# Performance work log

Hardware: AMD Instinct MI355X
Metric: run time of the kernel (lower is better)

## Reference

```python
import jax, jax.numpy as jnp
import numpy as np

FC = 16  # feat_channel
EPS = 1e-4


def _sch_forward(sch_feat, conv_weight, mask, target, pre_ind, ind):
    B, C, H, W = sch_feat.shape
    M = pre_ind.shape[1]
    fc = FC
    # _tranpose_and_gather_feat: gather per-object weight vectors at pre_ind
    cw = conv_weight.reshape(B, conv_weight.shape[1], H * W)          # B,Wt,HW
    weight = jnp.take_along_axis(cw, pre_ind[:, None, :], axis=2)    # B,Wt,M
    weight = jnp.transpose(weight, (0, 2, 1))                         # B,M,Wt
    # split into the 3-layer dynamic MLP params
    s1 = (fc + 2) * fc
    w1 = weight[..., :s1].reshape(B, M, fc, fc + 2)
    b1 = weight[..., s1:s1 + fc]
    s2 = s1 + fc
    w2 = weight[..., s2:s2 + fc * fc].reshape(B, M, fc, fc)
    b2 = weight[..., s2 + fc * fc:s2 + fc * fc + fc]
    s3 = s2 + fc * fc + fc
    w3 = weight[..., s3:s3 + fc]                                      # B,M,fc (1 out channel)
    b3 = weight[..., s3 + fc:s3 + fc + 1]                             # B,M,1
    # relative coordinate grids; note torch: x = pre_ind % w (int), y = pre_ind / w (true div)
    x = (pre_ind % W).astype(jnp.float32)
    y = pre_ind.astype(jnp.float32) / W
    xg = jnp.arange(W, dtype=jnp.float32)
    yg = jnp.arange(H, dtype=jnp.float32)
    x_rel = (xg[None, None, None, :] - x[:, :, None, None]) / 128.0   # B,M,1,W
    y_rel = (yg[None, None, :, None] - y[:, :, None, None]) / 128.0   # B,M,H,1
    x_rel = jnp.broadcast_to(x_rel, (B, M, H, W))
    y_rel = jnp.broadcast_to(y_rel, (B, M, H, W))
    feat = jnp.concatenate([
        jnp.broadcast_to(sch_feat[:, None], (B, M, C, H, W)),
        x_rel[:, :, None], y_rel[:, :, None]], axis=2)                # B,M,fc+2,H,W
    # three grouped 1x1 convs == per-instance matmuls
    h = jax.nn.relu(jnp.einsum('bmchw,bmoc->bmohw', feat, w1) + b1[:, :, :, None, None])
    h = jax.nn.relu(jnp.einsum('bmchw,bmoc->bmohw', h, w2) + b2[:, :, :, None, None])
    hm = jnp.einsum('bmchw,bmc->bmhw', h, w3) + b3[:, :, :, None]      # B,M,H,W
    hm = jnp.clip(jax.nn.sigmoid(hm), EPS, 1.0 - EPS)                  # _sigmoid
    # FastFocalLoss over (B*M, 1, H, W) with cat = 0
    neg_loss = jnp.sum(jnp.log(1.0 - hm) * hm ** 2 * (1.0 - target) ** 4)
    hm_flat = hm.reshape(B, M, H * W)
    pos_pred = jnp.take_along_axis(hm_flat, ind[..., None], axis=2)[..., 0]  # B,M
    pos_loss = jnp.sum(jnp.log(pos_pred) * (1.0 - pos_pred) ** 2 * mask)
    num_pos = jnp.sum(mask)
    loss = jnp.where(num_pos == 0,
                     -neg_loss,
                     -(pos_loss + neg_loss) / jnp.maximum(num_pos, 1.0))
    return loss


def setup_inputs() -> dict:
    key = jax.random.key(0)
    k1, k2, k3, k4, k5 = jax.random.split(key, 5)
    B, M, H, W = 4, 32, 152, 272
    Wt = (FC + 2) * FC + FC + FC * FC + FC + FC + 1  # 593
    return {
        'sch_feat': jax.random.normal(k1, (B, FC, H, W), dtype=jnp.float32),
        'conv_weight': jax.random.normal(k2, (B, Wt, H, W), dtype=jnp.float32),
        'mask': jnp.ones((B, M), dtype=jnp.float32),
        'pre_ind': jax.random.randint(k3, (B, M), 0, H * W, dtype=jnp.int64) if jax.config.jax_enable_x64 else jax.random.randint(k3, (B, M), 0, H * W).astype(jnp.int32),
        'target': jax.random.uniform(k4, (B, M, H, W), dtype=jnp.float32),
        'ind': jax.random.randint(k5, (B, M), 0, H * W).astype(jnp.int32),
    }


def reference(sch_feat, conv_weight, mask, pre_ind, target, ind):
    return _sch_forward(sch_feat, conv_weight, mask, target, pre_ind, ind)
```

## Files before the change

kernel.cpp:

```cpp
#include <hip/hip_runtime.h>

typedef unsigned int uint;
typedef unsigned short ushort;

constexpr int Bc = 4, Mc = 32, Hc = 152, Wc = 272;
constexpr int HWc = Hc * Wc;
constexpr int WTc = 593;
constexpr int NB = 8;
constexpr int NEG_BLOCKS = Bc * Mc * NB;
constexpr int ITERS = HWc / 64;
constexpr int POS_OFF = 1024;
constexpr int WC_OFF = 2048;
constexpr int WC_STRIDE = 600;
constexpr int APK1_OFF = WC_OFF + 128 * WC_STRIDE;
constexpr int APK2_OFF = APK1_OFF + 128 * 64 * 4;
constexpr size_t XOFF_BYTES = (size_t)(APK2_OFF + 128 * 64 * 4) * 4;
constexpr int CH = 24;
constexpr int XCVT_BLOCKS = 162 * Bc;

using f32x4 = __attribute__((ext_vector_type(4))) float;
using bf16x8 = __attribute__((ext_vector_type(8))) short;

__device__ inline uint pkbf(float lo, float hi) {
  uint r;
  asm("v_cvt_pk_bf16_f32 %0, %1, %2" : "=v"(r) : "v"(lo), "v"(hi));
  return r;
}
__device__ inline float bpermf(int byteaddr, float v) {
  return __int_as_float(__builtin_amdgcn_ds_bpermute(byteaddr, __float_as_int(v)));
}
__device__ inline uint bpermu(int byteaddr, uint v) {
  return (uint)__builtin_amdgcn_ds_bpermute(byteaddr, (int)v);
}

union FR { uint u[4]; bf16x8 v; };

__global__ __launch_bounds__(256) void fused_pre(const float* __restrict__ sf_all,
                                                 const float* __restrict__ cw,
                                                 const int* __restrict__ pre_ind,
                                                 const int* __restrict__ ind,
                                                 const float* __restrict__ mask,
                                                 ushort* __restrict__ xb,
                                                 float* __restrict__ ws) {
  __shared__ float sw[WTc];
  const int blk = blockIdx.x, tid = threadIdx.x;

  if (blk < XCVT_BLOCKS) {
    const int b = blk / 162, bx = blk - b * 162;
    const int px = bx * 256 + tid;
    if (px < HWc) {
      const float* s = sf_all + (size_t)b * 16 * HWc + px;
      uint q[8];
#pragma unroll
      for (int i = 0; i < 8; i++) q[i] = pkbf(s[(size_t)(2 * i) * HWc], s[(size_t)(2 * i + 1) * HWc]);
      const int hh = px / Wc, xx = px - hh * Wc;
      const uint q8 = pkbf((float)xx * 0.0078125f, (float)hh * 0.0078125f);
      uint4* dst = (uint4*)(xb + ((size_t)b * HWc + px) * CH);
      dst[0] = make_uint4(q[0], q[1], q[2], q[3]);
      dst[1] = make_uint4(q[4], q[5], q[6], q[7]);
      dst[2] = make_uint4(q8, 0u, 0u, 0u);
    }
    if (blk == 0 && tid < 32) ((uint*)(xb + (size_t)Bc * HWc * CH))[tid] = 0;
    return;
  }

  const int bm = blk - XCVT_BLOCKS, b = bm >> 5;
  const int p = pre_ind[bm];
  const float* wcol = cw + (size_t)b * WTc * HWc + p;
  float* wc = ws + WC_OFF + bm * WC_STRIDE;
  for (int j = tid; j < WTc; j += 256) {
    float v = wcol[(size_t)j * HWc];
    sw[j] = v;
    wc[j] = v;
  }
  __syncthreads();

  if (tid < 64) {
    const int g = tid >> 4, o = tid & 15;
    float a1f[8], a2f[8];
#pragma unroll
    for (int e = 0; e < 8; e++) {
      int k = 8 * g + e;
      a1f[e] = (k < 18) ? sw[o * 18 + k] : 0.0f;
      a2f[e] = (k < 16) ? sw[304 + o * 16 + k] : 0.0f;
    }
    uint4 u1, u2;
    u1.x = pkbf(a1f[0], a1f[1]); u1.y = pkbf(a1f[2], a1f[3]);
    u1.z = pkbf(a1f[4], a1f[5]); u1.w = pkbf(a1f[6], a1f[7]);
    u2.x = pkbf(a2f[0], a2f[1]); u2.y = pkbf(a2f[2], a2f[3]);
    u2.z = pkbf(a2f[4], a2f[5]); u2.w = pkbf(a2f[6], a2f[7]);
    ((uint4*)(ws + APK1_OFF))[bm * 64 + tid] = u1;
    ((uint4*)(ws + APK2_OFF))[bm * 64 + tid] = u2;
  } else if (tid == 64) {
    const float* sf = sf_all + (size_t)b * 16 * HWc;
    const int pi = ind[bm];
    float f[18];
#pragma unroll
    for (int c = 0; c < 16; c++) f[c] = sf[(size_t)c * HWc + pi];
    const int hh = pi / Wc;
    const float x0 = (float)(p % Wc);
    const float y0 = (float)p / (float)Wc;
    f[16] = ((float)(pi - hh * Wc) - x0) * 0.0078125f;
    f[17] = ((float)hh - y0) * 0.0078125f;
    float h1[16];
    for (int oo = 0; oo < 16; oo++) {
      float a = sw[288 + oo];
#pragma unroll
      for (int c = 0; c < 18; c++) a = fmaf(sw[oo * 18 + c], f[c], a);
      h1[oo] = fmaxf(a, 0.0f);
    }
    float h2[16];
    for (int oo = 0; oo < 16; oo++) {
      float a = sw[560 + oo];
#pragma unroll
      for (int c = 0; c < 16; c++) a = fmaf(sw[304 + oo * 16 + c], h1[c], a);
      h2[oo] = fmaxf(a, 0.0f);
    }
    float zv = sw[592];
#pragma unroll
    for (int c = 0; c < 16; c++) zv = fmaf(sw[576 + c], h2[c], zv);
    float hm = __fdividef(1.0f, 1.0f + __expf(-zv));
    hm = fminf(fmaxf(hm, 1e-4f), 1.0f - 1e-4f);
    const float om = 1.0f - hm;
    ws[POS_OFF + bm] = __logf(hm) * om * om * mask[bm];
  }
}

__global__ __launch_bounds__(256, 4) void sch_neg(const float* __restrict__ target,
                                                  const ushort* __restrict__ xbf,
                                                  const int* __restrict__ pre_ind,
                                                  float* __restrict__ ws) {
  const int tid = threadIdx.x;
  const int lane = tid & 63;
  const int wid = tid >> 6;
  const int xcd = blockIdx.x & 7;
  const int slot = blockIdx.x >> 3;
  const int b = xcd >> 1;
  const int m = slot & 31;
  const int nb = ((slot >> 5) << 1) | (xcd & 1);
  const int bm = (b << 5) | m;
  const int g = lane >> 4;
  const int o = lane & 15;

  const int p = pre_ind[bm];
  const float x0 = (float)(p % Wc);
  const float y0 = (float)p / (float)Wc;

  FR A1, A2;
  {
    uint4 u1 = ((const uint4*)(ws + APK1_OFF))[bm * 64 + lane];
    uint4 u2 = ((const uint4*)(ws + APK2_OFF))[bm * 64 + lane];
    A1.u[0] = u1.x; A1.u[1] = u1.y; A1.u[2] = u1.z; A1.u[3] = u1.w;
    A2.u[0] = u2.x; A2.u[1] = u2.y; A2.u[2] = u2.z; A2.u[3] = u2.w;
  }
  const float* wc = ws + WC_OFF + bm * WC_STRIDE;
  f32x4 c1v, c2v;
  float w3r[4];
#pragma unroll
  for (int r = 0; r < 4; r++) {
    int row = 4 * g + r;
    c1v[r] = wc[288 + row] - (wc[row * 18 + 16] * x0 + wc[row * 18 + 17] * y0) * 0.0078125f;
    c2v[r] = wc[560 + row];
    w3r[r] = wc[576 + row];
  }
  const float b3 = wc[592];

  const ushort* xb = xbf + (size_t)b * HWc * CH;
  const float* tg = target + (size_t)bm * HWc;

  const int aX16 = (lane ^ 16) << 2;
  const int aX32 = (lane ^ 32) << 2;
  const int aS0 = (o + ((g == 1) ? 32 : 0)) << 2;
  const int aS1 = (o + ((g == 1) ? 48 : 16)) << 2;

  float acc = 0.0f;
  const int gw = nb * 4 + wid;
  for (int it = gw; it < ITERS; it += 32) {
    const int base = it * 64;
    uint4 ld[4];
#pragma unroll
    for (int c = 0; c < 4; c++)
      ld[c] = *(const uint4*)(xb + (size_t)(base + 16 * c + o) * CH + g * 8);
    const float tval = tg[base + lane];

    float zpv[4];
#pragma unroll
    for (int half = 0; half < 2; half++) {
      FR B1a, B1b;
      B1a.u[0] = ld[2 * half].x; B1a.u[1] = ld[2 * half].y;
      B1a.u[2] = ld[2 * half].z; B1a.u[3] = ld[2 * half].w;
      B1b.u[0] = ld[2 * half + 1].x; B1b.u[1] = ld[2 * half + 1].y;
      B1b.u[2] = ld[2 * half + 1].z; B1b.u[3] = ld[2 * half + 1].w;
      f32x4 d1a = __builtin_amdgcn_mfma_f32_16x16x32_bf16(A1.v, B1a.v, c1v, 0, 0, 0);
      f32x4 d1b = __builtin_amdgcn_mfma_f32_16x16x32_bf16(A1.v, B1b.v, c1v, 0, 0, 0);
      uint pa0 = pkbf(fmaxf(d1a[0], 0.0f), fmaxf(d1a[1], 0.0f));
      uint pa1 = pkbf(fmaxf(d1a[2], 0.0f), fmaxf(d1a[3], 0.0f));
      uint pb0 = pkbf(fmaxf(d1b[0], 0.0f), fmaxf(d1b[1], 0.0f));
      uint pb1 = pkbf(fmaxf(d1b[2], 0.0f), fmaxf(d1b[3], 0.0f));
      FR B2a, B2b;
      B2a.u[0] = bpermu(aS0, pa0); B2a.u[1] = bpermu(aS0, pa1);
      B2a.u[2] = bpermu(aS1, pa0); B2a.u[3] = bpermu(aS1, pa1);
      B2b.u[0] = bpermu(aS0, pb0); B2b.u[1] = bpermu(aS0, pb1);
      B2b.u[2] = bpermu(aS1, pb0); B2b.u[3] = bpermu(aS1, pb1);
      f32x4 d2a = __builtin_amdgcn_mfma_f32_16x16x32_bf16(A2.v, B2a.v, c2v, 0, 0, 0);
      f32x4 d2b = __builtin_amdgcn_mfma_f32_16x16x32_bf16(A2.v, B2b.v, c2v, 0, 0, 0);
      zpv[2 * half] = fmaxf(d2a[0], 0.0f) * w3r[0] + fmaxf(d2a[1], 0.0f) * w3r[1] +
                      fmaxf(d2a[2], 0.0f) * w3r[2] + fmaxf(d2a[3], 0.0f) * w3r[3];
      zpv[2 * half + 1] = fmaxf(d2b[0], 0.0f) * w3r[0] + fmaxf(d2b[1], 0.0f) * w3r[1] +
                          fmaxf(d2b[2], 0.0f) * w3r[2] + fmaxf(d2b[3], 0.0f) * w3r[3];
    }
    const int b0 = g & 1, b1 = g & 2;
    const float pk_g  = b1 ? (b0 ? zpv[3] : zpv[2]) : (b0 ? zpv[1] : zpv[0]);
    const float pk_g1 = b1 ? (b0 ? zpv[2] : zpv[3]) : (b0 ? zpv[0] : zpv[1]);
    const float pk_g2 = b1 ? (b0 ? zpv[1] : zpv[0]) : (b0 ? zpv[3] : zpv[2]);
    const float pk_g3 = b1 ? (b0 ? zpv[0] : zpv[1]) : (b0 ? zpv[2] : zpv[3]);
    const float tA = pk_g + bpermf(aX16, pk_g1);
    const float tB = pk_g2 + bpermf(aX16, pk_g3);
    const float S = tA + bpermf(aX32, tB);

    const float zz = S + b3;
    float hm = __fdividef(1.0f, 1.0f + __expf(-zz));
    hm = fminf(fmaxf(hm, 1e-4f), 1.0f - 1e-4f);
    const float u = 1.0f - tval;
    const float u2 = u * u;
    acc += __logf(1.0f - hm) * hm * hm * (u2 * u2);
  }

  __shared__ float red[256];
  red[tid] = acc;
  __syncthreads();
  for (int s = 128; s > 0; s >>= 1) {
    if (tid < s) red[tid] += red[tid + s];
    __syncthreads();
  }
  if (tid == 0) ws[blockIdx.x] = red[0];
}

__global__ __launch_bounds__(256) void sch_final(const float* __restrict__ ws,
                                                 const float* __restrict__ mask,
                                                 float* __restrict__ out) {
  __shared__ float red[256];
  const int t = threadIdx.x;

  float s = 0.0f;
  for (int i = t; i < NEG_BLOCKS; i += 256) s += ws[i];
  red[t] = s; __syncthreads();
  for (int k = 128; k > 0; k >>= 1) { if (t < k) red[t] += red[t + k]; __syncthreads(); }
  const float neg = red[0];
  __syncthreads();

  float pv = (t < Bc * Mc) ? ws[POS_OFF + t] : 0.0f;
  red[t] = pv; __syncthreads();
  for (int k = 128; k > 0; k >>= 1) { if (t < k) red[t] += red[t + k]; __syncthreads(); }
  const float pos = red[0];
  __syncthreads();

  float mv = (t < Bc * Mc) ? mask[t] : 0.0f;
  red[t] = mv; __syncthreads();
  for (int k = 128; k > 0; k >>= 1) { if (t < k) red[t] += red[t + k]; __syncthreads(); }

  if (t == 0) {
    float np = red[0];
    out[0] = (np == 0.0f) ? (-neg) : (-(pos + neg) / fmaxf(np, 1.0f));
  }
}

extern "C" void kernel_launch(void* const* d_in, const int* in_sizes, int n_in,
                              void* d_out, int out_size, void* d_ws, size_t ws_size,
                              hipStream_t stream) {
  const float* sch_feat    = (const float*)d_in[0];
  const float* conv_weight = (const float*)d_in[1];
  const float* mask        = (const float*)d_in[2];
  const int*   pre_ind     = (const int*)d_in[3];
  const float* target      = (const float*)d_in[4];
  const int*   ind         = (const int*)d_in[5];
  float* out = (float*)d_out;
  float* ws  = (float*)d_ws;
  ushort* xbf = (ushort*)((char*)d_ws + XOFF_BYTES);

  fused_pre<<<dim3(XCVT_BLOCKS + Bc * Mc), dim3(256), 0, stream>>>(
      sch_feat, conv_weight, pre_ind, ind, mask, xbf, ws);
  sch_neg<<<dim3(NEG_BLOCKS), dim3(256), 0, stream>>>(target, xbf, pre_ind, ws);
  sch_final<<<dim3(1), dim3(256), 0, stream>>>(ws, mask, out);
}
```

Baseline: 49.16 us.

## Use grouped 16-pixel feature layout and software-prefetch next iteration loads

Reorganizes the bf16 feature buffer from per-pixel 48-byte records into 16-pixel groups, with channel halves and the coordinate channel stored contiguously, so each lane's load is coalesced and the padding lanes skip loads entirely. It also double-buffers the feature and target loads so the next iteration's data is fetched while the current one computes through the MFMA chain. The cost is extra registers for the prefetch buffers, which may affect occupancy under the 4-wave launch bound. Lanes in group 3 now read zeros and group 2 sees only the coordinate word, which must match the A-matrix packing.

```diff
diff --git a/kernel.cpp b/kernel.cpp
--- a/kernel.cpp
+++ b/kernel.cpp
@@ -2,6 +2,7 @@
 
 typedef unsigned int uint;
 typedef unsigned short ushort;
+typedef unsigned char uint8_t_;
 
 constexpr int Bc = 4, Mc = 32, Hc = 152, Wc = 272;
 constexpr int HWc = Hc * Wc;
@@ -15,7 +16,8 @@
 constexpr int APK1_OFF = WC_OFF + 128 * WC_STRIDE;
 constexpr int APK2_OFF = APK1_OFF + 128 * 64 * 4;
 constexpr size_t XOFF_BYTES = (size_t)(APK2_OFF + 128 * 64 * 4) * 4;
-constexpr int CH = 24;
+constexpr int GRPB = HWc / 16;
+constexpr int GSTRIDE = 576;
 constexpr int XCVT_BLOCKS = 162 * Bc;
 
 using f32x4 = __attribute__((ext_vector_type(4))) float;
@@ -40,7 +42,7 @@
                                                  const int* __restrict__ pre_ind,
                                                  const int* __restrict__ ind,
                                                  const float* __restrict__ mask,
-                                                 ushort* __restrict__ xb,
+                                                 unsigned char* __restrict__ xb,
                                                  float* __restrict__ ws) {
   __shared__ float sw[WTc];
   const int blk = blockIdx.x, tid = threadIdx.x;
@@ -55,12 +57,12 @@
       for (int i = 0; i < 8; i++) q[i] = pkbf(s[(size_t)(2 * i) * HWc], s[(size_t)(2 * i + 1) * HWc]);
       const int hh = px / Wc, xx = px - hh * Wc;
       const uint q8 = pkbf((float)xx * 0.0078125f, (float)hh * 0.0078125f);
-      uint4* dst = (uint4*)(xb + ((size_t)b * HWc + px) * CH);
-      dst[0] = make_uint4(q[0], q[1], q[2], q[3]);
-      dst[1] = make_uint4(q[4], q[5], q[6], q[7]);
-      dst[2] = make_uint4(q8, 0u, 0u, 0u);
-    }
-    if (blk == 0 && tid < 32) ((uint*)(xb + (size_t)Bc * HWc * CH))[tid] = 0;
+      const int grp = px >> 4, o = px & 15;
+      unsigned char* gb = xb + ((size_t)b * GRPB + grp) * GSTRIDE;
+      *(uint4*)(gb + o * 16) = make_uint4(q[0], q[1], q[2], q[3]);
+      *(uint4*)(gb + 256 + o * 16) = make_uint4(q[4], q[5], q[6], q[7]);
+      *(uint*)(gb + 512 + o * 4) = q8;
+    }
     return;
   }
 
@@ -127,7 +129,7 @@
 }
 
 __global__ __launch_bounds__(256, 4) void sch_neg(const float* __restrict__ target,
-                                                  const ushort* __restrict__ xbf,
+                                                  const unsigned char* __restrict__ xbf,
                                                   const int* __restrict__ pre_ind,
                                                   float* __restrict__ ws) {
   const int tid = threadIdx.x;
@@ -165,23 +167,38 @@
   }
   const float b3 = wc[592];
 
-  const ushort* xb = xbf + (size_t)b * HWc * CH;
+  const unsigned char* xb = xbf + (size_t)b * GRPB * GSTRIDE;
   const float* tg = target + (size_t)bm * HWc;
 
   const int aX16 = (lane ^ 16) << 2;
   const int aX32 = (lane ^ 32) << 2;
   const int aS0 = (o + ((g == 1) ? 32 : 0)) << 2;
   const int aS1 = (o + ((g == 1) ? 48 : 16)) << 2;
+  const int offA = (g << 8) + (o << 4);
+  const int offC = 512 + (o << 2);
+
+  auto loadB1 = [&](int grpidx, uint4& q) {
+    const unsigned char* gb = xb + (size_t)grpidx * GSTRIDE;
+    if (g < 2) q = *(const uint4*)(gb + offA);
+    else if (g == 2) q.x = *(const uint*)(gb + offC);
+  };
 
   float acc = 0.0f;
   const int gw = nb * 4 + wid;
+
+  uint4 ld[4];
+  float tval;
+#pragma unroll
+  for (int c = 0; c < 4; c++) { ld[c] = make_uint4(0, 0, 0, 0); loadB1(gw * 4 + c, ld[c]); }
+  tval = tg[gw * 64 + lane];
+
   for (int it = gw; it < ITERS; it += 32) {
-    const int base = it * 64;
-    uint4 ld[4];
-#pragma unroll
-    for (int c = 0; c < 4; c++)
-      ld[c] = *(const uint4*)(xb + (size_t)(base + 16 * c + o) * CH + g * 8);
-    const float tval = tg[base + lane];
+    const int nit = (it + 32 < ITERS) ? it + 32 : it;
+    uint4 ldn[4];
+    float tvn;
+#pragma unroll
+    for (int c = 0; c < 4; c++) { ldn[c] = make_uint4(0, 0, 0, 0); loadB1(nit * 4 + c, ldn[c]); }
+    tvn = tg[nit * 64 + lane];
 
     float zpv[4];
 #pragma unroll
@@ -224,6 +241,10 @@
     const float u = 1.0f - tval;
     const float u2 = u * u;
     acc += __logf(1.0f - hm) * hm * hm * (u2 * u2);
+
+#pragma unroll
+    for (int c = 0; c < 4; c++) ld[c] = ldn[c];
+    tval = tvn;
   }
 
   __shared__ float red[256];
@@ -276,7 +297,7 @@
   const int*   ind         = (const int*)d_in[5];
   float* out = (float*)d_out;
   float* ws  = (float*)d_ws;
-  ushort* xbf = (ushort*)((char*)d_ws + XOFF_BYTES);
+  unsigned char* xbf = (unsigned char*)d_ws + XOFF_BYTES;
 
   fused_pre<<<dim3(XCVT_BLOCKS + Bc * Mc), dim3(256), 0, stream>>>(
       sch_feat, conv_weight, pre_ind, ind, mask, xbf, ws);
```

New measurement: 51.35 us. 4.5% more time.
